# Optimization experiments

Hardware: AMD Instinct MI355X
Metric: run time of the kernel (lower is better)

## Reference

```python
import jax, jax.numpy as jnp
import numpy as np

WINDOW = 5
MAX_LEVELS = 4
EPS = 1e-6

_SX = (jnp.array([[-1., 0., 1.], [-2., 0., 2.], [-1., 0., 1.]], dtype=jnp.float32) / 8.0).reshape(1, 1, 3, 3)
_SY = jnp.transpose(_SX, (0, 1, 3, 2))
_DN = ('NCHW', 'OIHW', 'NCHW')


def _avg_pool2(x):
    B, C, H, W = x.shape
    return x.reshape(B, C, H // 2, 2, W // 2, 2).mean(axis=(3, 5))


def _warp(img, flow):
    # bilinear grid_sample, align_corners=True, zeros padding; sample at pixel coords grid+flow
    B, C, H, W = img.shape
    ys, xs = jnp.meshgrid(jnp.arange(H, dtype=img.dtype), jnp.arange(W, dtype=img.dtype), indexing='ij')
    x = xs[None] + flow[:, 0]  # [B,H,W]
    y = ys[None] + flow[:, 1]
    x0f, y0f = jnp.floor(x), jnp.floor(y)
    wx, wy = x - x0f, y - y0f
    imf = img.reshape(B, C, H * W)

    def gather(yi, xi):
        valid = (xi >= 0) & (xi <= W - 1) & (yi >= 0) & (yi <= H - 1)
        xi_c = jnp.clip(xi, 0, W - 1).astype(jnp.int32)
        yi_c = jnp.clip(yi, 0, H - 1).astype(jnp.int32)
        flat = (yi_c * W + xi_c).reshape(B, 1, H * W)
        v = jnp.take_along_axis(imf, jnp.broadcast_to(flat, (B, C, H * W)), axis=2).reshape(B, C, H, W)
        return v * valid[:, None].astype(img.dtype)

    out = (gather(y0f, x0f) * ((1 - wx) * (1 - wy))[:, None]
           + gather(y0f, x0f + 1) * (wx * (1 - wy))[:, None]
           + gather(y0f + 1, x0f) * ((1 - wx) * wy)[:, None]
           + gather(y0f + 1, x0f + 1) * (wx * wy)[:, None])
    return out


def _resize_ac(x, Hn, Wn):
    # bilinear resize, align_corners=True (static shapes)
    B, C, H, W = x.shape
    if (H, W) == (Hn, Wn):
        return x
    ys = jnp.linspace(0.0, H - 1, Hn, dtype=x.dtype)
    xs = jnp.linspace(0.0, W - 1, Wn, dtype=x.dtype)
    y0 = jnp.clip(jnp.floor(ys), 0, H - 2).astype(jnp.int32)
    x0 = jnp.clip(jnp.floor(xs), 0, W - 2).astype(jnp.int32)
    wy = (ys - y0)[None, None, :, None]
    wx = (xs - x0)[None, None, None, :]
    rows = x[:, :, y0, :] * (1 - wy) + x[:, :, y0 + 1, :] * wy
    return rows[:, :, :, x0] * (1 - wx) + rows[:, :, :, x0 + 1] * wx


def _lucas_kanade(I1, I2):
    if I1.shape[1] > 1:
        I1 = I1.mean(1, keepdims=True)
        I2 = I2.mean(1, keepdims=True)
    Ix = jax.lax.conv_general_dilated(I1, _SX, (1, 1), [(1, 1), (1, 1)], dimension_numbers=_DN)
    Iy = jax.lax.conv_general_dilated(I1, _SY, (1, 1), [(1, 1), (1, 1)], dimension_numbers=_DN)
    It = I2 - I1
    # stack all 5 structure-tensor products and box-filter them with one grouped conv
    stats = jnp.concatenate([Ix * Ix, Iy * Iy, Ix * Iy, Ix * It, Iy * It], axis=1)  # [B,5,H,W]
    boxk = jnp.ones((5, 1, WINDOW, WINDOW), dtype=I1.dtype)
    p0 = WINDOW // 2
    p1 = WINDOW - p0 - 1
    S = jax.lax.conv_general_dilated(stats, boxk, (1, 1), [(p0, p1), (p0, p1)],
                                     feature_group_count=5, dimension_numbers=_DN)
    Sxx, Syy, Sxy, Sxt, Syt = jnp.split(S, 5, axis=1)
    inv = 1.0 / (Sxx * Syy - Sxy * Sxy + EPS)
    u = (-Syy * Sxt + Sxy * Syt) * inv
    v = (Sxy * Sxt - Sxx * Syt) * inv
    return jnp.concatenate([u, v], axis=1)


def setup_inputs() -> dict:
    key = jax.random.key(0)
    k1, k2 = jax.random.split(key)
    img1 = jax.random.uniform(k1, (8, 3, 512, 512), dtype=jnp.float32)
    img2 = jax.random.uniform(k2, (8, 3, 512, 512), dtype=jnp.float32)
    return {"img1": img1, "img2": img2}


def reference(img1, img2):
    B, C, H, W = img1.shape
    levels = max(1, MAX_LEVELS)
    pyr1, pyr2 = [img1], [img2]
    for _ in range(1, levels):
        pyr1.append(_avg_pool2(pyr1[-1]))
        pyr2.append(_avg_pool2(pyr2[-1]))
    flow = jnp.zeros((B, 2, pyr1[-1].shape[2], pyr1[-1].shape[3]), dtype=img1.dtype)
    for lvl in range(levels - 1, -1, -1):
        I1, I2 = pyr1[lvl], pyr2[lvl]
        if lvl < levels - 1:
            flow = _resize_ac(flow, I1.shape[2], I1.shape[3]) * 2.0
        I2w = _warp(I2, flow)
        flow = flow + _lucas_kanade(I1, I2w)
    if flow.shape[2:] != (H, W):
        fh, fw = flow.shape[2], flow.shape[3]
        flow = _resize_ac(flow, H, W)
        flow = flow * jnp.array([W / fw, H / fh], dtype=flow.dtype).reshape(1, 2, 1, 1)
    return flow
```

## Files before the change

kernel.cpp:

```cpp
#include <hip/hip_runtime.h>

#define NB 8

typedef float f2 __attribute__((ext_vector_type(2)));

__global__ __launch_bounds__(256) void gray_pyr_kernel(
    const float* __restrict__ img1, const float* __restrict__ img2,
    float* __restrict__ g0a, float* __restrict__ g0b,
    float* __restrict__ g1a, float* __restrict__ g1b,
    float* __restrict__ g2a, float* __restrict__ g2b,
    float* __restrict__ g3a, float* __restrict__ g3b) {
    const int W = 512, HW = 512 * 512;
    __shared__ float sL1a[16][17], sL1b[16][17];
    __shared__ float sL2a[8][9], sL2b[8][9];

    int blk = blockIdx.x;
    int b = blk % NB;
    int t = blk / NB;
    int ty = t / 16, tx = t % 16;
    int lx = threadIdx.x % 16, ly = threadIdx.x / 16;
    int y1 = ty * 16 + ly, x1 = tx * 16 + lx;

    size_t base = (size_t)b * 3 * HW + (size_t)(2 * y1) * W + 2 * x1;
    const float third = 1.0f / 3.0f;

    f2 a0c0 = __builtin_nontemporal_load((const f2*)(img1 + base));
    f2 a1c0 = __builtin_nontemporal_load((const f2*)(img1 + base + W));
    f2 a0c1 = __builtin_nontemporal_load((const f2*)(img1 + base + HW));
    f2 a1c1 = __builtin_nontemporal_load((const f2*)(img1 + base + HW + W));
    f2 a0c2 = __builtin_nontemporal_load((const f2*)(img1 + base + 2 * HW));
    f2 a1c2 = __builtin_nontemporal_load((const f2*)(img1 + base + 2 * HW + W));
    float p00 = (a0c0.x + a0c1.x + a0c2.x) * third;
    float p01 = (a0c0.y + a0c1.y + a0c2.y) * third;
    float p10 = (a1c0.x + a1c1.x + a1c2.x) * third;
    float p11 = (a1c0.y + a1c1.y + a1c2.y) * third;
    size_t gbase = (size_t)b * HW + (size_t)(2 * y1) * W + 2 * x1;
    *(f2*)(g0a + gbase) = (f2){p00, p01};
    *(f2*)(g0a + gbase + W) = (f2){p10, p11};
    float pa = (p00 + p01 + p10 + p11) * 0.25f;
    g1a[(size_t)b * 256 * 256 + y1 * 256 + x1] = pa;
    sL1a[ly][lx] = pa;

    f2 b0c0 = __builtin_nontemporal_load((const f2*)(img2 + base));
    f2 b1c0 = __builtin_nontemporal_load((const f2*)(img2 + base + W));
    f2 b0c1 = __builtin_nontemporal_load((const f2*)(img2 + base + HW));
    f2 b1c1 = __builtin_nontemporal_load((const f2*)(img2 + base + HW + W));
    f2 b0c2 = __builtin_nontemporal_load((const f2*)(img2 + base + 2 * HW));
    f2 b1c2 = __builtin_nontemporal_load((const f2*)(img2 + base + 2 * HW + W));
    float q00 = (b0c0.x + b0c1.x + b0c2.x) * third;
    float q01 = (b0c0.y + b0c1.y + b0c2.y) * third;
    float q10 = (b1c0.x + b1c1.x + b1c2.x) * third;
    float q11 = (b1c0.y + b1c1.y + b1c2.y) * third;
    *(f2*)(g0b + gbase) = (f2){q00, q01};
    *(f2*)(g0b + gbase + W) = (f2){q10, q11};
    float pb = (q00 + q01 + q10 + q11) * 0.25f;
    g1b[(size_t)b * 256 * 256 + y1 * 256 + x1] = pb;
    sL1b[ly][lx] = pb;
    __syncthreads();

    if (threadIdx.x < 64) {
        int y2 = threadIdx.x / 8, x2 = threadIdx.x % 8;
        float va = (sL1a[2 * y2][2 * x2] + sL1a[2 * y2][2 * x2 + 1]
                  + sL1a[2 * y2 + 1][2 * x2] + sL1a[2 * y2 + 1][2 * x2 + 1]) * 0.25f;
        float vb = (sL1b[2 * y2][2 * x2] + sL1b[2 * y2][2 * x2 + 1]
                  + sL1b[2 * y2 + 1][2 * x2] + sL1b[2 * y2 + 1][2 * x2 + 1]) * 0.25f;
        g2a[(size_t)b * 128 * 128 + (ty * 8 + y2) * 128 + tx * 8 + x2] = va;
        g2b[(size_t)b * 128 * 128 + (ty * 8 + y2) * 128 + tx * 8 + x2] = vb;
        sL2a[y2][x2] = va;
        sL2b[y2][x2] = vb;
    }
    __syncthreads();

    if (threadIdx.x < 16) {
        int y3 = threadIdx.x / 4, x3 = threadIdx.x % 4;
        float va = (sL2a[2 * y3][2 * x3] + sL2a[2 * y3][2 * x3 + 1]
                  + sL2a[2 * y3 + 1][2 * x3] + sL2a[2 * y3 + 1][2 * x3 + 1]) * 0.25f;
        float vb = (sL2b[2 * y3][2 * x3] + sL2b[2 * y3][2 * x3 + 1]
                  + sL2b[2 * y3 + 1][2 * x3] + sL2b[2 * y3 + 1][2 * x3 + 1]) * 0.25f;
        g3a[(size_t)b * 64 * 64 + (ty * 4 + y3) * 64 + tx * 4 + x3] = va;
        g3b[(size_t)b * 64 * 64 + (ty * 4 + y3) * 64 + tx * 4 + x3] = vb;
    }
}

template <int MODE, int H, int W, int TH>
__device__ __forceinline__ void lk_strip(
    int b, int tix, const float* __restrict__ g1, const float* __restrict__ g2,
    const float* __restrict__ fin, float* __restrict__ fout) {
    constexpr int XT = (W + 57) / 58;
    constexpr int NR = TH + 4;
    constexpr int Hs = H / 2, Ws = W / 2;
    constexpr float scale = (float)(Hs - 1) / (float)(H - 1);

    const int lane = threadIdx.x & 63;
    const int xt = tix % XT, yt = tix / XT;
    const int x = xt * 58 - 3 + lane;
    const bool xin = (x >= 0) && (x < W);

    const float* G1 = g1 + (size_t)b * H * W;
    const float* G2 = g2 + (size_t)b * H * W;
    float* FO = fout + (size_t)b * 2 * H * W;

    const int p0 = yt * TH - 2;

    auto issue1 = [&](int yy) -> float {
        return (xin && yy >= 0 && yy < H) ? G1[yy * W + x] : 0.0f;
    };
    auto dands = [&](float gv, float& d, float& s) {
        float gl = __shfl_up(gv, 1);
        float gr = __shfl_down(gv, 1);
        d = gr - gl;
        s = gl + 2.0f * gv + gr;
    };
    auto hs5 = [&](float v) {
        float a = __shfl_down(v, 1);
        float c = __shfl_down(v, 2);
        float t = v + a + c;
        return __shfl_up(t, 2) + a + c;
    };

    float g[NR + 2];
#pragma unroll
    for (int j = 0; j < NR + 2; ++j) g[j] = issue1(p0 - 1 + j);

    float i2d[MODE ? 1 : NR];
    if (!MODE) {
#pragma unroll
        for (int i = 0; i < NR; ++i) {
            int yc = p0 + i;
            i2d[i] = (xin && yc >= 0 && yc < H) ? G2[yc * W + x] : 0.0f;
        }
    }

    float su[MODE ? NR : 1], sv[MODE ? NR : 1];
    f2 wt[MODE ? NR : 1], wb[MODE ? NR : 1];
    if (MODE) {
        const float* FU = fin + (size_t)b * 2 * Hs * Ws;
        const float* FV = FU + Hs * Ws;
        float sx = (float)x * scale;
        int cx0 = min(max((int)sx, 0), Ws - 2);
        float wxf = sx - (float)cx0;
        int y0cur = min(max((int)((float)p0 * scale), 0), Hs - 2);
        f2 cu0, cu1, cv0, cv1;
        __builtin_memcpy(&cu0, FU + y0cur * Ws + cx0, 8);
        __builtin_memcpy(&cu1, FU + (y0cur + 1) * Ws + cx0, 8);
        __builtin_memcpy(&cv0, FV + y0cur * Ws + cx0, 8);
        __builtin_memcpy(&cv1, FV + (y0cur + 1) * Ws + cx0, 8);
#pragma unroll
        for (int i = 0; i < NR; ++i) {
            int yc = p0 + i;
            int y0i = min(max((int)((float)yc * scale), 0), Hs - 2);
            if (y0i != y0cur) {
                cu0 = cu1; cv0 = cv1;
                __builtin_memcpy(&cu1, FU + (y0i + 1) * Ws + cx0, 8);
                __builtin_memcpy(&cv1, FV + (y0i + 1) * Ws + cx0, 8);
                y0cur = y0i;
            }
            float wyf = (float)yc * scale - (float)y0cur;
            float ut = cu0.x + (cu1.x - cu0.x) * wyf;
            float ub = cu0.y + (cu1.y - cu0.y) * wyf;
            float vt = cv0.x + (cv1.x - cv0.x) * wyf;
            float vb = cv0.y + (cv1.y - cv0.y) * wyf;
            su[i] = 2.0f * (ut + (ub - ut) * wxf);
            sv[i] = 2.0f * (vt + (vb - vt) * wxf);
            float xx = (float)x + su[i], yy2 = (float)yc + sv[i];
            int xi = (int)floorf(xx), yi = (int)floorf(yy2);
            int xl = min(max(xi, 0), W - 2);
            int ya = min(max(yi, 0), H - 1), yb2 = min(max(yi + 1, 0), H - 1);
            __builtin_memcpy(&wt[i], G2 + ya * W + xl, 8);
            __builtin_memcpy(&wb[i], G2 + yb2 * W + xl, 8);
        }
    }

    float hxx[5], hyy[5], hxy[5], hxt[5], hyt[5];
#pragma unroll
    for (int k = 0; k < 5; ++k) { hxx[k] = hyy[k] = hxy[k] = hxt[k] = hyt[k] = 0.0f; }

    float dm, d0, sm, s0, dp, sp;
    dands(g[0], dm, sm);
    dands(g[1], d0, s0);

#pragma unroll
    for (int i = 0; i < NR; ++i) {
        const int yc = p0 + i;
        dands(g[i + 2], dp, sp);
        float Ix = (dm + 2.0f * d0 + dp) * 0.125f;
        float Iy = (sp - sm) * 0.125f;

        float I2w;
        if (MODE) {
            float xx = (float)x + su[i], yy2 = (float)yc + sv[i];
            float x0f = floorf(xx), y0f = floorf(yy2);
            float wx = xx - x0f, wy = yy2 - y0f;
            int xi = (int)x0f, yi = (int)y0f;
            int xl = min(max(xi, 0), W - 2);
            bool t0 = (xi == xl);
            float v00 = t0 ? wt[i].x : wt[i].y;
            float v01 = t0 ? wt[i].y : wt[i].x;
            float v10 = t0 ? wb[i].x : wb[i].y;
            float v11 = t0 ? wb[i].y : wb[i].x;
            float mx0 = (xi >= 0 && xi < W) ? 1.0f : 0.0f;
            float mx1 = (xi >= -1 && xi < W - 1) ? 1.0f : 0.0f;
            float my0 = (yi >= 0 && yi < H) ? 1.0f : 0.0f;
            float my1 = (yi >= -1 && yi < H - 1) ? 1.0f : 0.0f;
            I2w = v00 * ((1.0f - wx) * (1.0f - wy) * mx0 * my0)
                + v01 * (wx * (1.0f - wy) * mx1 * my0)
                + v10 * ((1.0f - wx) * wy * mx0 * my1)
                + v11 * (wx * wy * mx1 * my1);
        } else {
            I2w = i2d[i];
        }
        float It = I2w - g[i + 1];
        float vm = (xin && yc >= 0 && yc < H) ? 1.0f : 0.0f;
        Ix *= vm; Iy *= vm; It *= vm;

        const int k = i % 5;
        hxx[k] = Ix * Ix;
        hyy[k] = Iy * Iy;
        hxy[k] = Ix * Iy;
        hxt[k] = Ix * It;
        hyt[k] = Iy * It;

        if (i >= 4) {
            float vxx = hxx[0] + hxx[1] + hxx[2] + hxx[3] + hxx[4];
            float vyy = hyy[0] + hyy[1] + hyy[2] + hyy[3] + hyy[4];
            float vxy = hxy[0] + hxy[1] + hxy[2] + hxy[3] + hxy[4];
            float vxt = hxt[0] + hxt[1] + hxt[2] + hxt[3] + hxt[4];
            float vyt = hyt[0] + hyt[1] + hyt[2] + hyt[3] + hyt[4];
            float Sxx = hs5(vxx);
            float Syy = hs5(vyy);
            float Sxy = hs5(vxy);
            float Sxt = hs5(vxt);
            float Syt = hs5(vyt);
            float inv = 1.0f / (Sxx * Syy - Sxy * Sxy + 1e-6f);
            float du = (-Syy * Sxt + Sxy * Syt) * inv;
            float dv = (Sxy * Sxt - Sxx * Syt) * inv;
            int yo = yc - 2;
            if (lane >= 3 && lane <= 60 && x < W) {
                float ou = du, ov = dv;
                if (MODE) { ou += su[i - 2]; ov += sv[i - 2]; }
                FO[yo * W + x] = ou;
                FO[H * W + yo * W + x] = ov;
            }
        }
        dm = d0; d0 = dp;
        sm = s0; s0 = sp;
    }
}

template <int MODE, int H, int W, int TH>
__global__ __launch_bounds__(256, 4) void lk_roll(
    const float* __restrict__ g1, const float* __restrict__ g2,
    const float* __restrict__ fin, float* __restrict__ fout) {
    constexpr int XT = (W + 57) / 58;
    constexpr int TILES = XT * (H / TH);
    const int wid = threadIdx.x >> 6;
    const int b = blockIdx.x % NB;
    const int tix = (blockIdx.x / NB) * 4 + wid;
    if (tix >= TILES) return;
    lk_strip<MODE, H, W, TH>(b, tix, g1, g2, fin, fout);
}

extern "C" void kernel_launch(void* const* d_in, const int* in_sizes, int n_in,
                              void* d_out, int out_size, void* d_ws, size_t ws_size,
                              hipStream_t stream) {
    const float* img1 = (const float*)d_in[0];
    const float* img2 = (const float*)d_in[1];
    float* out = (float*)d_out;
    float* ws = (float*)d_ws;

    constexpr size_t HW0 = 512 * 512, HW1 = 256 * 256, HW2 = 128 * 128, HW3 = 64 * 64;
    constexpr size_t TOT = NB * (HW0 + HW1 + HW2 + HW3);
    float* p1 = ws;
    float* p2 = ws + TOT;
    float* f64 = p2 + TOT;
    float* f128 = f64 + NB * 2 * HW3;
    float* f256 = f128 + NB * 2 * HW2;
    float* p1_0 = p1, * p1_1 = p1 + NB * HW0, * p1_2 = p1_1 + NB * HW1, * p1_3 = p1_2 + NB * HW2;
    float* p2_0 = p2, * p2_1 = p2 + NB * HW0, * p2_2 = p2_1 + NB * HW1, * p2_3 = p2_2 + NB * HW2;

    gray_pyr_kernel<<<NB * 256, 256, 0, stream>>>(
        img1, img2, p1_0, p2_0, p1_1, p2_1, p1_2, p2_2, p1_3, p2_3);

    {
        constexpr int tiles = 2 * 64;
        lk_roll<0, 64, 64, 1><<<NB * ((tiles + 3) / 4), 256, 0, stream>>>(p1_3, p2_3, nullptr, f64);
    }
    {
        constexpr int tiles = 3 * 128;
        lk_roll<1, 128, 128, 1><<<NB * ((tiles + 3) / 4), 256, 0, stream>>>(p1_2, p2_2, f64, f128);
    }
    {
        constexpr int tiles = 5 * 128;
        lk_roll<1, 256, 256, 2><<<NB * ((tiles + 3) / 4), 256, 0, stream>>>(p1_1, p2_1, f128, f256);
    }
    {
        constexpr int tiles = 9 * 128;
        lk_roll<1, 512, 512, 4><<<NB * ((tiles + 3) / 4), 256, 0, stream>>>(p1_0, p2_0, f256, out);
    }
}
```

Measured before the change: 59.58 us.

## Warp gather via wave shuffles from preloaded G2 rows when displacement is small

```diff
diff --git a/kernel.cpp b/kernel.cpp
--- a/kernel.cpp
+++ b/kernel.cpp
@@ -93,7 +93,8 @@
 
     const int lane = threadIdx.x & 63;
     const int xt = tix % XT, yt = tix / XT;
-    const int x = xt * 58 - 3 + lane;
+    const int xb = xt * 58 - 3;
+    const int x = xb + lane;
     const bool xin = (x >= 0) && (x < W);
 
     const float* G1 = g1 + (size_t)b * H * W;
@@ -122,17 +123,26 @@
 #pragma unroll
     for (int j = 0; j < NR + 2; ++j) g[j] = issue1(p0 - 1 + j);
 
-    float i2d[MODE ? 1 : NR];
+    float g2w[MODE ? NR + 4 : 1];
+    if (MODE) {
+        int xc = min(max(x, 0), W - 1);
+#pragma unroll
+        for (int j = 0; j < NR + 4; ++j) {
+            int row = min(max(p0 - 2 + j, 0), H - 1);
+            g2w[j] = G2[row * W + xc];
+        }
+    }
+
+    float i2w[NR];
     if (!MODE) {
 #pragma unroll
         for (int i = 0; i < NR; ++i) {
             int yc = p0 + i;
-            i2d[i] = (xin && yc >= 0 && yc < H) ? G2[yc * W + x] : 0.0f;
+            i2w[i] = (xin && yc >= 0 && yc < H) ? G2[yc * W + x] : 0.0f;
         }
     }
 
     float su[MODE ? NR : 1], sv[MODE ? NR : 1];
-    f2 wt[MODE ? NR : 1], wb[MODE ? NR : 1];
     if (MODE) {
         const float* FU = fin + (size_t)b * 2 * Hs * Ws;
         const float* FV = FU + Hs * Ws;
@@ -162,12 +172,51 @@
             float vb = cv0.y + (cv1.y - cv0.y) * wyf;
             su[i] = 2.0f * (ut + (ub - ut) * wxf);
             sv[i] = 2.0f * (vt + (vb - vt) * wxf);
+
             float xx = (float)x + su[i], yy2 = (float)yc + sv[i];
-            int xi = (int)floorf(xx), yi = (int)floorf(yy2);
-            int xl = min(max(xi, 0), W - 2);
-            int ya = min(max(yi, 0), H - 1), yb2 = min(max(yi + 1, 0), H - 1);
-            __builtin_memcpy(&wt[i], G2 + ya * W + xl, 8);
-            __builtin_memcpy(&wb[i], G2 + yb2 * W + xl, 8);
+            float x0f = floorf(xx), y0f = floorf(yy2);
+            float wx = xx - x0f, wy = yy2 - y0f;
+            int xi = (int)x0f, yi = (int)y0f;
+            int dyi = yi - yc;
+            int li = xi - xb;
+            bool ok = (li >= 0) && (li <= 62) && (xi >= 0) && (xi <= W - 2)
+                   && (dyi >= -2) && (dyi <= 1) && (yi >= 0) && (yi <= H - 2);
+            int dy0 = __builtin_amdgcn_readfirstlane(dyi);
+            bool uni = __all(ok && (dyi == dy0));
+            if (uni) {
+                float A, B;
+                if (dy0 == -2)      { A = g2w[i];     B = g2w[i + 1]; }
+                else if (dy0 == -1) { A = g2w[i + 1]; B = g2w[i + 2]; }
+                else if (dy0 == 0)  { A = g2w[i + 2]; B = g2w[i + 3]; }
+                else                { A = g2w[i + 3]; B = g2w[i + 4]; }
+                float v00 = __shfl(A, li);
+                float v01 = __shfl(A, li + 1);
+                float v10 = __shfl(B, li);
+                float v11 = __shfl(B, li + 1);
+                i2w[i] = v00 * ((1.0f - wx) * (1.0f - wy))
+                       + v01 * (wx * (1.0f - wy))
+                       + v10 * ((1.0f - wx) * wy)
+                       + v11 * (wx * wy);
+            } else {
+                int xl = min(max(xi, 0), W - 2);
+                int ya = min(max(yi, 0), H - 1), yb2 = min(max(yi + 1, 0), H - 1);
+                f2 wtv, wbv;
+                __builtin_memcpy(&wtv, G2 + ya * W + xl, 8);
+                __builtin_memcpy(&wbv, G2 + yb2 * W + xl, 8);
+                bool t0 = (xi == xl);
+                float v00 = t0 ? wtv.x : wtv.y;
+                float v01 = t0 ? wtv.y : wtv.x;
+                float v10 = t0 ? wbv.x : wbv.y;
+                float v11 = t0 ? wbv.y : wbv.x;
+                float mx0 = (xi >= 0 && xi < W) ? 1.0f : 0.0f;
+                float mx1 = (xi >= -1 && xi < W - 1) ? 1.0f : 0.0f;
+                float my0 = (yi >= 0 && yi < H) ? 1.0f : 0.0f;
+                float my1 = (yi >= -1 && yi < H - 1) ? 1.0f : 0.0f;
+                i2w[i] = v00 * ((1.0f - wx) * (1.0f - wy) * mx0 * my0)
+                       + v01 * (wx * (1.0f - wy) * mx1 * my0)
+                       + v10 * ((1.0f - wx) * wy * mx0 * my1)
+                       + v11 * (wx * wy * mx1 * my1);
+            }
         }
     }
 
@@ -185,31 +234,7 @@
         dands(g[i + 2], dp, sp);
         float Ix = (dm + 2.0f * d0 + dp) * 0.125f;
         float Iy = (sp - sm) * 0.125f;
-
-        float I2w;
-        if (MODE) {
-            float xx = (float)x + su[i], yy2 = (float)yc + sv[i];
-            float x0f = floorf(xx), y0f = floorf(yy2);
-            float wx = xx - x0f, wy = yy2 - y0f;
-            int xi = (int)x0f, yi = (int)y0f;
-            int xl = min(max(xi, 0), W - 2);
-            bool t0 = (xi == xl);
-            float v00 = t0 ? wt[i].x : wt[i].y;
-            float v01 = t0 ? wt[i].y : wt[i].x;
-            float v10 = t0 ? wb[i].x : wb[i].y;
-            float v11 = t0 ? wb[i].y : wb[i].x;
-            float mx0 = (xi >= 0 && xi < W) ? 1.0f : 0.0f;
-            float mx1 = (xi >= -1 && xi < W - 1) ? 1.0f : 0.0f;
-            float my0 = (yi >= 0 && yi < H) ? 1.0f : 0.0f;
-            float my1 = (yi >= -1 && yi < H - 1) ? 1.0f : 0.0f;
-            I2w = v00 * ((1.0f - wx) * (1.0f - wy) * mx0 * my0)
-                + v01 * (wx * (1.0f - wy) * mx1 * my0)
-                + v10 * ((1.0f - wx) * wy * mx0 * my1)
-                + v11 * (wx * wy * mx1 * my1);
-        } else {
-            I2w = i2d[i];
-        }
-        float It = I2w - g[i + 1];
+        float It = i2w[i] - g[i + 1];
         float vm = (xin && yc >= 0 && yc < H) ? 1.0f : 0.0f;
         Ix *= vm; Iy *= vm; It *= vm;
 
```

Result: no change. 59.17 us (median of 2 runs) (-0.7%).
